# Kernel tuning notes

Hardware: AMD Instinct MI355X
Metric: run time of the kernel (lower is better)

## Reference

```python
import jax, jax.numpy as jnp
import numpy as np

SEQ, PREV, BS, D_IN, H, D = 512, 512, 8, 1024, 16, 64


def setup_inputs() -> dict:
    key = jax.random.key(0)
    ks = jax.random.split(key, 10)
    s = 0.02
    inp = {
        "input_": jax.random.normal(ks[0], (SEQ, BS, D_IN), jnp.float32),
        "pos_embs": jax.random.normal(ks[1], (SEQ + PREV, D_IN), jnp.float32),
        "memory": jax.random.normal(ks[2], (PREV, BS, D_IN), jnp.float32),
        "u": jax.random.normal(ks[3], (H, D), jnp.float32) * s,
        "v": jax.random.normal(ks[4], (H, D), jnp.float32) * s,
        # causal mask allowing full attention to memory: triu with diagonal=1+prev
        "mask": (jnp.triu(jnp.ones((SEQ, SEQ + PREV), jnp.bool_), k=1 + PREV))[..., None],
        "W_kv": jax.random.normal(ks[5], (D_IN, 2 * H * D), jnp.float32) * s,
        "W_q": jax.random.normal(ks[6], (D_IN, H * D), jnp.float32) * s,
        "W_p": jax.random.normal(ks[7], (D_IN, H * D), jnp.float32) * s,
        "W_out": jax.random.normal(ks[8], (H * D, D_IN), jnp.float32) * s,
        "ln_gamma": jnp.ones((D_IN,), jnp.float32),
        "ln_beta": jnp.zeros((D_IN,), jnp.float32),
    }
    return inp


def _rel_shift(x):
    # x: (q, k, bs, H) -> pad one zero column, reshape-transpose trick, drop first row
    q, k, bs, h = x.shape
    zp = jnp.zeros((q, 1, bs, h), x.dtype)
    return jnp.concatenate([zp, x], axis=1).reshape(k + 1, q, bs, h)[1:].reshape(q, k, bs, h)


def reference(input_, pos_embs, memory, u, v, mask, W_kv, W_q, W_p, W_out, ln_gamma, ln_beta):
    cur_seq, bs, d_in = input_.shape
    prev_seq = memory.shape[0]
    tot = cur_seq + prev_seq
    h, d = u.shape
    scale = 1.0 / d ** 0.5

    iwm = jnp.concatenate([memory, input_], axis=0)          # (tot, bs, d_in)
    kv = jnp.einsum('jbe,ef->jbf', iwm, W_kv)                 # (tot, bs, 2*H*d)
    k_t, v_t = jnp.split(kv, 2, axis=-1)
    q_t = jnp.einsum('ibe,ef->ibf', input_, W_q)              # (cur, bs, H*d)

    q4 = q_t.reshape(cur_seq, bs, h, d)
    k4 = k_t.reshape(tot, bs, h, d)
    v4 = v_t.reshape(tot, bs, h, d)

    content_attn = jnp.einsum('ibhd,jbhd->ijbh', q4 + u, k4)  # (cur, tot, bs, H)

    p_t = (pos_embs @ W_p).reshape(tot, h, d)                 # (tot, H, d)
    position_attn = jnp.einsum('ibhd,jhd->ijbh', q4 + v, p_t)
    position_attn = _rel_shift(position_attn)

    attn = content_attn + position_attn
    attn = jnp.where(mask[..., None], -jnp.inf, attn)         # mask: (cur, tot, 1) -> (cur, tot, 1, 1)
    attn = jax.nn.softmax(attn * scale, axis=1)

    awv = jnp.einsum('ijbh,jbhd->ibhd', attn, v4).reshape(cur_seq, bs, h * d)
    out = input_ + awv @ W_out                                # residual

    mu = jnp.mean(out, axis=-1, keepdims=True)
    var = jnp.mean((out - mu) ** 2, axis=-1, keepdims=True)
    out = (out - mu) / jnp.sqrt(var + 1e-5) * ln_gamma + ln_beta
    return out
```

## Files before the change

kernel.cpp:

```cpp
#include <hip/hip_runtime.h>
#include <math.h>

#define SEQ  512
#define PREV 512
#define TOT  1024
#define BSZ  8
#define DIN  1024
#define NH   16
#define HD   64

typedef __bf16 bf16;
typedef __bf16 bf16x8 __attribute__((ext_vector_type(8)));
typedef float  f32x4  __attribute__((ext_vector_type(4)));
typedef float  f32x16 __attribute__((ext_vector_type(16)));
typedef unsigned int u32;
typedef u32 u32x2 __attribute__((ext_vector_type(2)));

__device__ __forceinline__ f32x4 MFMA16(bf16x8 a, bf16x8 b, f32x4 c) {
    return __builtin_amdgcn_mfma_f32_16x16x32_bf16(a, b, c, 0, 0, 0);
}
__device__ __forceinline__ f32x16 MFMA32(bf16x8 a, bf16x8 b, f32x16 c) {
    return __builtin_amdgcn_mfma_f32_32x32x16_bf16(a, b, c, 0, 0, 0);
}

#define GLOAD16(g, l) __builtin_amdgcn_global_load_lds( \
    (const __attribute__((address_space(1))) void*)(g), \
    (__attribute__((address_space(3))) void*)(l), 16, 0, 0)

__device__ __forceinline__ unsigned short bfbits(float x) {
    return __builtin_bit_cast(unsigned short, (bf16)x);
}
__device__ __forceinline__ float bf2f(u32 bits16) {
    return __builtin_bit_cast(float, bits16 << 16);
}
__device__ __forceinline__ float exp2_raw(float x) {
    float r;
    asm("v_exp_f32 %0, %1" : "=v"(r) : "v"(x));
    return r;
}

__global__ __launch_bounds__(256) void prep_all(
    const float* __restrict__ memory, const float* __restrict__ input_,
    const float* __restrict__ pos,
    const float* __restrict__ W_kv, const float* __restrict__ W_q,
    const float* __restrict__ W_p,  const float* __restrict__ W_out,
    bf16* __restrict__ iwm, bf16* __restrict__ posb,
    bf16* __restrict__ wkv, bf16* __restrict__ wq,
    bf16* __restrict__ wp,  bf16* __restrict__ wo)
{
    __shared__ float tile[32][33];
    const int bid = blockIdx.x;
    const int t = threadIdx.x;
    if (bid < 9216) {
        const float* src; bf16* dst; int e4;
        if (bid < 8192) {
            e4 = (bid * 256 + t) * 4;
            src = (e4 < 4194304) ? memory : input_ - 4194304;
            dst = iwm;
        } else {
            e4 = ((bid - 8192) * 256 + t) * 4;
            src = pos; dst = posb;
        }
        float4 x = *(const float4*)(src + e4);
        union { bf16 h[4]; ushort4 u4; } pk;
        pk.h[0] = (bf16)x.x; pk.h[1] = (bf16)x.y; pk.h[2] = (bf16)x.z; pk.h[3] = (bf16)x.w;
        *(ushort4*)(dst + e4) = pk.u4;
        return;
    }
    const int rem = bid - 9216;
    const int bx = rem % 160, by = rem / 160;
    const float* W; bf16* Wt; int N, bn;
    if (bx < 64)       { W = W_kv;  Wt = wkv; N = 2048; bn = bx * 32; }
    else if (bx < 96)  { W = W_q;   Wt = wq;  N = 1024; bn = (bx - 64) * 32; }
    else if (bx < 128) { W = W_p;   Wt = wp;  N = 1024; bn = (bx - 96) * 32; }
    else               { W = W_out; Wt = wo;  N = 1024; bn = (bx - 128) * 32; }
    const int bk = by * 32;
    const int r = t >> 3, c4 = (t & 7) * 4;
    float4 x = *(const float4*)(W + (size_t)(bk + r) * N + bn + c4);
    tile[r][c4 + 0] = x.x; tile[r][c4 + 1] = x.y;
    tile[r][c4 + 2] = x.z; tile[r][c4 + 3] = x.w;
    __syncthreads();
    union { bf16 h[4]; ushort4 u4; } pk;
#pragma unroll
    for (int i = 0; i < 4; ++i) pk.h[i] = (bf16)tile[c4 + i][r];
    *(ushort4*)(Wt + (size_t)(bn + r) * 1024 + bk + c4) = pk.u4;
}

__global__ __launch_bounds__(256, 1) void gemm_kv(
    const bf16* __restrict__ A, const bf16* __restrict__ Bt,
    bf16* __restrict__ C, int M, int N, int K)
{
    __shared__ __align__(16) bf16 A_s[2][256 * 64];
    __shared__ __align__(16) bf16 B_s[2][256 * 64];
    const int t = threadIdx.x;
    const int w = t >> 6, lane = t & 63;
    const int ql = lane & 31, hi2 = lane >> 5;
    const int wm = w >> 1, wn = w & 1;
    const int lin = blockIdx.y * 8 + blockIdx.x;
    const int xcd = lin & 7, idx = lin >> 3;
    const int bm = (xcd * 4 + (idx & 3)) * 256;
    const int bn = (idx >> 2) * 256;

    f32x16 acc[4][4];
#pragma unroll
    for (int mf = 0; mf < 4; ++mf)
#pragma unroll
        for (int nf = 0; nf < 4; ++nf) acc[mf][nf] = (f32x16){};

    const int l7 = lane & 7, l3 = lane >> 3;

    auto stage_half = [&](int buf, int ks, int h) {
        const bf16* __restrict__ src = (h < 2) ? A : Bt;
        const int base = (h < 2) ? bm : bn;
        const int hh = (h & 1) * 128;
        bf16* dst = (h < 2) ? &A_s[buf][0] : &B_s[buf][0];
        const int k0 = ks << 6;
#pragma unroll
        for (int g = 0; g < 4; ++g) {
            const int row = hh + g * 32 + 8 * w + l3;
            const bf16* gp = src + (size_t)(base + row) * K + k0 + ((l7 ^ (row & 7)) * 8);
            GLOAD16(gp, dst + (size_t)row * 64 + l7 * 8);
        }
    };

    bf16x8 af[2][4], bfr[2][4];
    auto LDA = [&](int buf, int kt, int set) {
#pragma unroll
        for (int mf = 0; mf < 4; ++mf) {
            int row = wm * 128 + mf * 32 + ql;
            af[set][mf] = *(const bf16x8*)&A_s[buf][(size_t)row * 64 + (((kt * 2 + hi2) ^ (row & 7)) * 8)];
        }
    };
    auto LDB = [&](int buf, int kt, int set) {
#pragma unroll
        for (int nf = 0; nf < 4; ++nf) {
            int row = wn * 128 + nf * 32 + ql;
            bfr[set][nf] = *(const bf16x8*)&B_s[buf][(size_t)row * 64 + (((kt * 2 + hi2) ^ (row & 7)) * 8)];
        }
    };

    stage_half(0, 0, 0); stage_half(0, 0, 1); stage_half(0, 0, 2); stage_half(0, 0, 3);

    const int nk = K >> 6;
    for (int ks = 0; ks < nk; ++ks) {
        const int cur = ks & 1, nxt = cur ^ 1;
        asm volatile("s_waitcnt vmcnt(0)" ::: "memory");
        __builtin_amdgcn_sched_barrier(0);
        __builtin_amdgcn_s_barrier();
        __builtin_amdgcn_sched_barrier(0);
        LDA(cur, 0, 0); LDB(cur, 0, 0);
        if (ks + 1 < nk) {
            stage_half(nxt, ks + 1, 0); stage_half(nxt, ks + 1, 1);
            stage_half(nxt, ks + 1, 2); stage_half(nxt, ks + 1, 3);
        }
#pragma unroll
        for (int kt = 0; kt < 4; ++kt) {
            const int set = kt & 1;
            if (kt < 3) {
                LDA(cur, kt + 1, set ^ 1); LDB(cur, kt + 1, set ^ 1);
                asm volatile("s_waitcnt lgkmcnt(8)" ::: "memory");
            } else {
                asm volatile("s_waitcnt lgkmcnt(0)" ::: "memory");
            }
            __builtin_amdgcn_sched_barrier(0);
            __builtin_amdgcn_s_setprio(1);
#pragma unroll
            for (int mf = 0; mf < 4; ++mf)
#pragma unroll
                for (int nf = 0; nf < 4; ++nf)
                    acc[mf][nf] = MFMA32(af[set][mf], bfr[set][nf], acc[mf][nf]);
            __builtin_amdgcn_s_setprio(0);
        }
    }

#pragma unroll
    for (int mf = 0; mf < 4; ++mf)
#pragma unroll
        for (int nf = 0; nf < 4; ++nf)
#pragma unroll
            for (int r = 0; r < 16; ++r) {
                int row = bm + wm * 128 + mf * 32 + (r & 3) + 8 * (r >> 2) + 4 * hi2;
                int col = bn + wn * 128 + nf * 32 + ql;
                C[(size_t)row * N + col] = (bf16)acc[mf][nf][r];
            }
}

__global__ __launch_bounds__(256) void gemm_out(
    const bf16* __restrict__ A, const bf16* __restrict__ Bt,
    const float* __restrict__ Rres, float* __restrict__ Cf, int N, int K)
{
    __shared__ __align__(16) bf16 A_s[2][128 * 64];
    __shared__ __align__(16) bf16 B_s[2][128 * 64];
    const int t = threadIdx.x;
    const int w = t >> 6, lane = t & 63;
    const int li = lane & 15, hi = lane >> 4;
    const int wr = w >> 1, wc = w & 1;
    const int bm = blockIdx.y * 128, bn = blockIdx.x * 128;
    const int l3 = lane >> 3, l7 = lane & 7;
    const int srcoct = ((l7 ^ l3) * 8);

    f32x4 acc[4][4];
#pragma unroll
    for (int m = 0; m < 4; ++m)
#pragma unroll
        for (int n = 0; n < 4; ++n) acc[m][n] = (f32x4){0.f, 0.f, 0.f, 0.f};

    auto stage = [&](int buf, int k0) {
#pragma unroll
        for (int i = 0; i < 4; ++i) {
            int c = w * 4 + i;
            GLOAD16(A + (size_t)(bm + c * 8 + l3) * K + k0 + srcoct, &A_s[buf][c * 512]);
            GLOAD16(Bt + (size_t)(bn + c * 8 + l3) * K + k0 + srcoct, &B_s[buf][c * 512]);
        }
    };

    stage(0, 0);
    const int nk = K >> 6;
    for (int ks = 0; ks < nk; ++ks) {
        const int cur = ks & 1, nxt = cur ^ 1;
        asm volatile("s_waitcnt vmcnt(0)" ::: "memory");
        __builtin_amdgcn_sched_barrier(0);
        __builtin_amdgcn_s_barrier();
        __builtin_amdgcn_sched_barrier(0);
        if (ks + 1 < nk) stage(nxt, (ks + 1) << 6);
#pragma unroll
        for (int kk = 0; kk < 2; ++kk) {
            bf16x8 af[4], bfr[4];
#pragma unroll
            for (int m = 0; m < 4; ++m) {
                int row = wr * 64 + m * 16 + li;
                af[m] = *(const bf16x8*)&A_s[cur][row * 64 + ((kk * 32 + hi * 8) ^ ((row & 7) * 8))];
            }
#pragma unroll
            for (int n = 0; n < 4; ++n) {
                int row = wc * 64 + n * 16 + li;
                bfr[n] = *(const bf16x8*)&B_s[cur][row * 64 + ((kk * 32 + hi * 8) ^ ((row & 7) * 8))];
            }
            asm volatile("s_waitcnt lgkmcnt(0)" ::: "memory");
            __builtin_amdgcn_sched_barrier(0);
            __builtin_amdgcn_s_setprio(1);
#pragma unroll
            for (int m = 0; m < 4; ++m)
#pragma unroll
                for (int n = 0; n < 4; ++n)
                    acc[m][n] = MFMA16(af[m], bfr[n], acc[m][n]);
            __builtin_amdgcn_s_setprio(0);
        }
    }

#pragma unroll
    for (int m = 0; m < 4; ++m)
#pragma unroll
        for (int n = 0; n < 4; ++n)
#pragma unroll
            for (int r = 0; r < 4; ++r) {
                int row = bm + wr * 64 + m * 16 + hi * 4 + r;
                int col = bn + wc * 64 + n * 16 + li;
                size_t off = (size_t)row * N + col;
                Cf[off] = acc[m][n][r] + Rres[off];
            }
}

__global__ __launch_bounds__(256) void gemm_qp(
    const bf16* __restrict__ iwmq, const bf16* __restrict__ posb,
    const bf16* __restrict__ wq, const bf16* __restrict__ wp,
    bf16* __restrict__ qbf, bf16* __restrict__ pbf)
{
    __shared__ __align__(16) bf16 A_s[128 * 64];
    __shared__ __align__(16) bf16 B_s[128 * 64];
    const int t = threadIdx.x;
    const int w = t >> 6, lane = t & 63;
    const int li = lane & 15, hi = lane >> 4;
    const int wr = w >> 1, wc = w & 1;
    const int by = blockIdx.y;
    const bf16* A; const bf16* Bt; bf16* Cb; int bm;
    if (by < 32) { A = iwmq; Bt = wq; Cb = qbf; bm = by * 128; }
    else         { A = posb; Bt = wp; Cb = pbf; bm = (by - 32) * 128; }
    const int bn = blockIdx.x * 128;
    const int l3 = lane >> 3, l7 = lane & 7;
    const int srcoct = ((l7 ^ l3) * 8);

    f32x4 acc[4][4];
#pragma unroll
    for (int m = 0; m < 4; ++m)
#pragma unroll
        for (int n = 0; n < 4; ++n) acc[m][n] = (f32x4){0.f, 0.f, 0.f, 0.f};

    auto stage = [&](int k0) {
#pragma unroll
        for (int i = 0; i < 4; ++i) {
            int c = w * 4 + i;
            GLOAD16(A + (size_t)(bm + c * 8 + l3) * 1024 + k0 + srcoct, &A_s[c * 512]);
            GLOAD16(Bt + (size_t)(bn + c * 8 + l3) * 1024 + k0 + srcoct, &B_s[c * 512]);
        }
    };

    stage(0);
    for (int ks = 0; ks < 16; ++ks) {
        __syncthreads();
#pragma unroll
        for (int kk = 0; kk < 2; ++kk) {
            bf16x8 af[4], bfr[4];
#pragma unroll
            for (int m = 0; m < 4; ++m) {
                int row = wr * 64 + m * 16 + li;
                af[m] = *(const bf16x8*)&A_s[row * 64 + ((kk * 32 + hi * 8) ^ ((row & 7) * 8))];
            }
#pragma unroll
            for (int n = 0; n < 4; ++n) {
                int row = wc * 64 + n * 16 + li;
                bfr[n] = *(const bf16x8*)&B_s[row * 64 + ((kk * 32 + hi * 8) ^ ((row & 7) * 8))];
            }
#pragma unroll
            for (int m = 0; m < 4; ++m)
#pragma unroll
                for (int n = 0; n < 4; ++n)
                    acc[m][n] = MFMA16(af[m], bfr[n], acc[m][n]);
        }
        __syncthreads();
        if (ks + 1 < 16) stage((ks + 1) << 6);
    }

#pragma unroll
    for (int m = 0; m < 4; ++m)
#pragma unroll
        for (int n = 0; n < 4; ++n)
#pragma unroll
            for (int r = 0; r < 4; ++r) {
                int row = bm + wr * 64 + m * 16 + hi * 4 + r;
                int col = bn + wc * 64 + n * 16 + li;
                Cb[(size_t)row * 1024 + col] = (bf16)acc[m][n][r];
            }
}

__global__ __launch_bounds__(256, 2) void attn_mfma(
    const bf16* __restrict__ kv, const bf16* __restrict__ qb,
    const bf16* __restrict__ pb, const float* __restrict__ u,
    const float* __restrict__ v, bf16* __restrict__ awv)
{
    const int bi = (blockIdx.z & 1) ? (3 - blockIdx.x) : blockIdx.x;
    const int i0 = bi * 128;
    const int b  = blockIdx.y;
    const int h  = blockIdx.z;
    const int t  = threadIdx.x;
    const int w  = t >> 6;
    const int lane = t & 63;
    const int ql  = lane & 31;
    const int hi2 = lane >> 5;

    __shared__ __align__(16) bf16 K_s[64 * 64];
    __shared__ __align__(16) bf16 V_s[64][72];
    __shared__ __align__(16) bf16 P_s[256 * 64];
    __shared__ __align__(16) char SCR[4][6912];

    char* rsc = SCR[w];

    const int c8 = t & 7;
    const int rq = t >> 3;
    const int nt = 2 * bi + 10;
    const int C0 = 384 - i0;
    const float SCL2 = 0.125f * 1.44269504088896f;

    bf16x8 vreg[2];
#pragma unroll
    for (int p = 0; p < 2; ++p)
        vreg[p] = *(const bf16x8*)(kv + (size_t)((p * 32 + rq) * BSZ + b) * 2048 + 1024 + h * HD + c8 * 8);
#pragma unroll
    for (int p = 0; p < 2; ++p)
        GLOAD16(kv + (size_t)((p * 32 + rq) * BSZ + b) * 2048 + h * HD + ((c8 ^ (rq & 7)) * 8),
                K_s + (p * 32 + rq) * 64 + c8 * 8);
#pragma unroll
    for (int cp = 0; cp < 6; ++cp) {
        int grow = C0 + cp * 32 + rq;
        GLOAD16(pb + (size_t)grow * DIN + h * HD + ((c8 ^ (rq & 7)) * 8),
                P_s + (grow & 255) * 64 + c8 * 8);
    }

    bf16x8 qu[4], qv[4];
    {
        const size_t qoff = ((size_t)(i0 + w * 32 + ql) * BSZ + b) * DIN + h * HD;
#pragma unroll
        for (int kk = 0; kk < 4; ++kk) {
            bf16x8 q8 = *(const bf16x8*)(qb + qoff + kk * 16 + hi2 * 8);
            const float* up = u + h * HD + kk * 16 + hi2 * 8;
            const float* vp = v + h * HD + kk * 16 + hi2 * 8;
#pragma unroll
            for (int m = 0; m < 8; ++m) {
                float qf = (float)q8[m];
                qu[kk][m] = (bf16)(qf + up[m]);
                qv[kk][m] = (bf16)(qf + vp[m]);
            }
        }
    }

    float mrun = -1e30f, lrun = 0.f;
    f32x16 o[2];
    o[0] = (f32x16){}; o[1] = (f32x16){};

    const int phq = (31 - ql) & 3;
    const int sel = phq >> 1;
    const int shb = (phq & 1) * 16;

    for (int tt = 0; tt < nt; ++tt) {
        const int j0 = tt * 64;

        __builtin_amdgcn_s_barrier();
        __builtin_amdgcn_sched_barrier(0);

#pragma unroll
        for (int p = 0; p < 2; ++p) {
            int j = p * 32 + rq;
#pragma unroll
            for (int mm = 0; mm < 8; ++mm)
                V_s[c8 * 8 + mm][(j + 8 * c8) & 63] = vreg[p][mm];
        }
        asm volatile("s_waitcnt vmcnt(0) lgkmcnt(0)" ::: "memory");
        __builtin_amdgcn_sched_barrier(0);
        __builtin_amdgcn_s_barrier();
        __builtin_amdgcn_sched_barrier(0);

        f32x16 st[2];
        st[0] = (f32x16){}; st[1] = (f32x16){};
        __builtin_amdgcn_s_setprio(1);
#pragma unroll
        for (int jt = 0; jt < 2; ++jt) {
            int row = jt * 32 + ql;
#pragma unroll
            for (int kk = 0; kk < 4; ++kk) {
                bf16x8 kf = *(const bf16x8*)&K_s[row * 64 + (((kk * 2 + hi2) ^ (ql & 7)) * 8)];
                st[jt] = MFMA32(kf, qu[kk], st[jt]);
            }
        }
        const int bwg = j0 - i0 + 480 - 32 * w;
        f32x16 rp[3];
        rp[0] = (f32x16){}; rp[1] = (f32x16){}; rp[2] = (f32x16){};
#pragma unroll
        for (int Rt = 0; Rt < 3; ++Rt) {
            int ring = (bwg + Rt * 32 + ql) & 255;
#pragma unroll
            for (int kk = 0; kk < 4; ++kk) {
                bf16x8 pf = *(const bf16x8*)&P_s[ring * 64 + (((kk * 2 + hi2) ^ (ring & 7)) * 8)];
                rp[Rt] = MFMA32(pf, qv[kk], rp[Rt]);
            }
        }
        __builtin_amdgcn_s_setprio(0);

#pragma unroll
        for (int Rt = 0; Rt < 3; ++Rt)
#pragma unroll
            for (int a = 0; a < 4; ++a) {
                u32 lo = (u32)bfbits(rp[Rt][a * 4 + 0]) | ((u32)bfbits(rp[Rt][a * 4 + 1]) << 16);
                u32 hi = (u32)bfbits(rp[Rt][a * 4 + 2]) | ((u32)bfbits(rp[Rt][a * 4 + 3]) << 16);
                *(u32x2*)(rsc + ql * 216 + 64 * Rt + 16 * a + 8 * hi2) = (u32x2){lo, hi};
            }

        __builtin_amdgcn_s_barrier();
        __builtin_amdgcn_sched_barrier(0);

        if (tt + 1 < nt) {
            const int j0n = j0 + 64;
#pragma unroll
            for (int p = 0; p < 2; ++p)
                vreg[p] = *(const bf16x8*)(kv + (size_t)((j0n + p * 32 + rq) * BSZ + b) * 2048 + 1024 + h * HD + c8 * 8);
#pragma unroll
            for (int p = 0; p < 2; ++p)
                GLOAD16(kv + (size_t)((j0n + p * 32 + rq) * BSZ + b) * 2048 + h * HD + ((c8 ^ (rq & 7)) * 8),
                        K_s + (p * 32 + rq) * 64 + c8 * 8);
        }
        if (tt + 3 < nt) {
            const int Cs = C0 + (tt + 3) * 64;
#pragma unroll
            for (int p = 0; p < 2; ++p) {
                int grow = Cs + p * 32 + rq;
                GLOAD16(pb + (size_t)grow * DIN + h * HD + ((c8 ^ (rq & 7)) * 8),
                        P_s + (grow & 255) * 64 + c8 * 8);
            }
        }

        float rowmax = -1e30f;
        const int limb = i0 + 32 * w + ql + PREV - j0;
        auto assemble = [&](bool domask) {
#pragma unroll
            for (int jt = 0; jt < 2; ++jt)
#pragma unroll
                for (int a = 0; a < 4; ++a) {
                    int e = jt * 32 + 8 * a + 4 * hi2 + 31 - ql;
                    const u32x2* W = (const u32x2*)(rsc + ql * 216 + 8 * (e >> 2));
                    u32x2 A0 = W[0], A1 = W[1];
                    u32 U0 = sel ? A0[1] : A0[0];
                    u32 U1 = sel ? A1[0] : A0[1];
                    u32 U2 = sel ? A1[1] : A1[0];
                    u32 o0 = (u32)((((unsigned long long)U1 << 32) | U0) >> shb);
                    u32 o1 = (u32)((((unsigned long long)U2 << 32) | U1) >> shb);
                    float pq[4] = {bf2f(o0 & 0xffffu), bf2f(o0 >> 16),
                                   bf2f(o1 & 0xffffu), bf2f(o1 >> 16)};
#pragma unroll
                    for (int rr = 0; rr < 4; ++rr) {
                        int r = a * 4 + rr;
                        int lj = jt * 32 + 8 * a + 4 * hi2 + rr;
                        float sv = (st[jt][r] + pq[rr]) * SCL2;
                        if (domask && lj > limb) sv = -1e30f;
                        st[jt][r] = sv;
                        rowmax = fmaxf(rowmax, sv);
                    }
                }
        };
        if (__builtin_amdgcn_readfirstlane(j0 + 63 - (i0 + 32 * w + PREV)) > 0)
            assemble(true);
        else
            assemble(false);

        {
            u32 rm = __builtin_bit_cast(u32, rowmax), rm2 = rm;
            asm("v_permlane32_swap_b32 %0, %1" : "+v"(rm), "+v"(rm2));
            rowmax = fmaxf(rowmax, __builtin_bit_cast(float, rm));
            rowmax = fmaxf(rowmax, __builtin_bit_cast(float, rm2));
        }

        if (!__all(rowmax - mrun <= 11.54f)) {
            float newm = fmaxf(mrun, rowmax);
            float fsc = exp2_raw(mrun - newm);
#pragma unroll
            for (int r = 0; r < 16; ++r) {
                float fr = __shfl(fsc, (r & 3) + 8 * (r >> 2) + 4 * hi2);
                o[0][r] *= fr; o[1][r] *= fr;
            }
            lrun *= fsc;
            mrun = newm;
        }
        float rowsum = 0.f;
#pragma unroll
        for (int jt = 0; jt < 2; ++jt)
#pragma unroll
            for (int r = 0; r < 16; ++r) {
                float p = exp2_raw(st[jt][r] - mrun);
                st[jt][r] = p;
                rowsum += p;
            }
        {
            u32 rs = __builtin_bit_cast(u32, rowsum), rs2 = rs;
            asm("v_permlane32_swap_b32 %0, %1" : "+v"(rs), "+v"(rs2));
            rowsum += __builtin_bit_cast(float, rs2);
        }
        lrun += rowsum;

        u32 pk0[2][4], pk1[2][4];
#pragma unroll
        for (int jt = 0; jt < 2; ++jt)
#pragma unroll
            for (int a = 0; a < 4; ++a) {
                pk0[jt][a] = (u32)bfbits(st[jt][a * 4 + 0]) | ((u32)bfbits(st[jt][a * 4 + 1]) << 16);
                pk1[jt][a] = (u32)bfbits(st[jt][a * 4 + 2]) | ((u32)bfbits(st[jt][a * 4 + 3]) << 16);
            }

        __builtin_amdgcn_s_setprio(1);
#pragma unroll
        for (int js = 0; js < 4; ++js) {
            const int jt = js >> 1, a0 = 2 * (js & 1), a1 = a0 + 1;
            u32 w0 = pk0[jt][a0], w2 = pk0[jt][a1];
            asm("v_permlane32_swap_b32 %0, %1" : "+v"(w0), "+v"(w2));
            u32 w1 = pk1[jt][a0], w3 = pk1[jt][a1];
            asm("v_permlane32_swap_b32 %0, %1" : "+v"(w1), "+v"(w3));
            union { u32 uw[4]; bf16x8 vv; } pa;
            pa.uw[0] = w0; pa.uw[1] = w1; pa.uw[2] = w2; pa.uw[3] = w3;
#pragma unroll
            for (int dt = 0; dt < 2; ++dt) {
                int dcol = dt * 32 + ql;
                int colb = (js * 16 + hi2 * 8 + 8 * (dcol >> 3)) & 63;
                bf16x8 vf = *(const bf16x8*)&V_s[dcol][colb];
                o[dt] = MFMA32(pa.vv, vf, o[dt]);
            }
        }
        __builtin_amdgcn_s_setprio(0);
    }

    float linv = __builtin_amdgcn_rcpf(lrun);
    float lr[16];
#pragma unroll
    for (int r = 0; r < 16; ++r) lr[r] = __shfl(linv, (r & 3) + 8 * (r >> 2) + 4 * hi2);
#pragma unroll
    for (int dt = 0; dt < 2; ++dt)
#pragma unroll
        for (int r = 0; r < 16; ++r) {
            int row = i0 + 32 * w + (r & 3) + 8 * (r >> 2) + 4 * hi2;
            awv[((size_t)row * BSZ + b) * DIN + h * HD + dt * 32 + ql] = (bf16)(o[dt][r] * lr[r]);
        }
}

__global__ __launch_bounds__(256) void ln_f32(
    float* __restrict__ out, const float* __restrict__ gamma, const float* __restrict__ beta)
{
    const int row = blockIdx.x;
    const int t = threadIdx.x;
    float4 x = *(float4*)(out + (size_t)row * DIN + t * 4);
    float s  = x.x + x.y + x.z + x.w;
    float ss = x.x * x.x + x.y * x.y + x.z * x.z + x.w * x.w;
#pragma unroll
    for (int wd = 1; wd < 64; wd <<= 1) { s += __shfl_xor(s, wd); ss += __shfl_xor(ss, wd); }
    __shared__ float sbuf[4], ssbuf[4];
    const int wave = t >> 6, lanei = t & 63;
    if (lanei == 0) { sbuf[wave] = s; ssbuf[wave] = ss; }
    __syncthreads();
    s  = sbuf[0] + sbuf[1] + sbuf[2] + sbuf[3];
    ss = ssbuf[0] + ssbuf[1] + ssbuf[2] + ssbuf[3];
    const float mu   = s * (1.f / DIN);
    const float var  = ss * (1.f / DIN) - mu * mu;
    const float rstd = rsqrtf(var + 1e-5f);
    float4 g  = *(const float4*)(gamma + t * 4);
    float4 bb = *(const float4*)(beta + t * 4);
    float4 y;
    y.x = (x.x - mu) * rstd * g.x + bb.x;
    y.y = (x.y - mu) * rstd * g.y + bb.y;
    y.z = (x.z - mu) * rstd * g.z + bb.z;
    y.w = (x.w - mu) * rstd * g.w + bb.w;
    *(float4*)(out + (size_t)row * DIN + t * 4) = y;
}

extern "C" void kernel_launch(void* const* d_in, const int* in_sizes, int n_in,
                              void* d_out, int out_size, void* d_ws, size_t ws_size,
                              hipStream_t stream)
{
    const float* input_ = (const float*)d_in[0];
    const float* pos    = (const float*)d_in[1];
    const float* memory = (const float*)d_in[2];
    const float* u      = (const float*)d_in[3];
    const float* v      = (const float*)d_in[4];
    const float* W_kv   = (const float*)d_in[6];
    const float* W_q    = (const float*)d_in[7];
    const float* W_p    = (const float*)d_in[8];
    const float* W_out  = (const float*)d_in[9];
    const float* gamma  = (const float*)d_in[10];
    const float* beta   = (const float*)d_in[11];

    bf16* iwm  = (bf16*)d_ws;
    bf16* kvb  = iwm  + (size_t)8192 * 1024;
    bf16* qbf  = kvb  + (size_t)8192 * 2048;
    bf16* pbf  = qbf  + (size_t)4096 * 1024;
    bf16* posb = pbf  + (size_t)1024 * 1024;
    bf16* wkv  = posb + (size_t)1024 * 1024;
    bf16* wq   = wkv  + (size_t)2048 * 1024;
    bf16* wp   = wq   + (size_t)1024 * 1024;
    bf16* wo   = wp   + (size_t)1024 * 1024;
    bf16* awvb = wo   + (size_t)1024 * 1024;
    float* outf = (float*)d_out;

    prep_all<<<14336, 256, 0, stream>>>(memory, input_, pos, W_kv, W_q, W_p, W_out,
                                        iwm, posb, wkv, wq, wp, wo);

    gemm_kv<<<dim3(8, 32), 256, 0, stream>>>(iwm, wkv, kvb, 8192, 2048, 1024);
    gemm_qp<<<dim3(8, 40), 256, 0, stream>>>(iwm + (size_t)4096 * 1024, posb, wq, wp, qbf, pbf);

    attn_mfma<<<dim3(4, 8, 16), 256, 0, stream>>>(kvb, qbf, pbf, u, v, awvb);

    gemm_out<<<dim3(8, 32), 256, 0, stream>>>(awvb, wo, input_, outf, 1024, 1024);
    ln_f32<<<4096, 256, 0, stream>>>(outf, gamma, beta);
}
```

Before: 170.0 us.

## Merge KV, Q and P projection GEMMs into one triple-buffered 512-thread kernel

Replaces the separate gemm_kv and gemm_qp launches with a single gemm_proj kernel of 336 blocks. Each block computes a 256x256 tile with 8 waves, using 16x16 MFMAs and K-steps of 32 staged through a 3-deep LDS ring with partial vmcnt waits. The aim is to fill the GPU in one wave of blocks, drop a launch and the tail between the two GEMMs, and overlap global loads better. The cost is smaller K-steps, more barriers per unit of work, and higher register pressure from a 32-fragment accumulator at 2 blocks per CU.

New measurement: 192.7 us. 13.3% more time.

```diff
diff --git a/kernel.cpp b/kernel.cpp
--- a/kernel.cpp
+++ b/kernel.cpp
@@ -86,102 +86,104 @@
     *(ushort4*)(Wt + (size_t)(bn + r) * 1024 + bk + c4) = pk.u4;
 }
 
-__global__ __launch_bounds__(256, 1) void gemm_kv(
-    const bf16* __restrict__ A, const bf16* __restrict__ Bt,
-    bf16* __restrict__ C, int M, int N, int K)
+__global__ __launch_bounds__(512, 2) void gemm_proj(
+    const bf16* __restrict__ iwm, const bf16* __restrict__ posb,
+    const bf16* __restrict__ wkv, const bf16* __restrict__ wq,
+    const bf16* __restrict__ wp,
+    bf16* __restrict__ kvb, bf16* __restrict__ qbf, bf16* __restrict__ pbf)
 {
-    __shared__ __align__(16) bf16 A_s[2][256 * 64];
-    __shared__ __align__(16) bf16 B_s[2][256 * 64];
+    __shared__ __align__(16) bf16 A_s[3][256 * 32];
+    __shared__ __align__(16) bf16 B_s[3][256 * 32];
     const int t = threadIdx.x;
     const int w = t >> 6, lane = t & 63;
-    const int ql = lane & 31, hi2 = lane >> 5;
-    const int wm = w >> 1, wn = w & 1;
-    const int lin = blockIdx.y * 8 + blockIdx.x;
-    const int xcd = lin & 7, idx = lin >> 3;
-    const int bm = (xcd * 4 + (idx & 3)) * 256;
-    const int bn = (idx >> 2) * 256;
-
-    f32x16 acc[4][4];
-#pragma unroll
-    for (int mf = 0; mf < 4; ++mf)
-#pragma unroll
-        for (int nf = 0; nf < 4; ++nf) acc[mf][nf] = (f32x16){};
-
-    const int l7 = lane & 7, l3 = lane >> 3;
-
-    auto stage_half = [&](int buf, int ks, int h) {
-        const bf16* __restrict__ src = (h < 2) ? A : Bt;
-        const int base = (h < 2) ? bm : bn;
-        const int hh = (h & 1) * 128;
-        bf16* dst = (h < 2) ? &A_s[buf][0] : &B_s[buf][0];
-        const int k0 = ks << 6;
-#pragma unroll
-        for (int g = 0; g < 4; ++g) {
-            const int row = hh + g * 32 + 8 * w + l3;
-            const bf16* gp = src + (size_t)(base + row) * K + k0 + ((l7 ^ (row & 7)) * 8);
-            GLOAD16(gp, dst + (size_t)row * 64 + l7 * 8);
+    const int li = lane & 15, hi = lane >> 4;
+    const int wm = w >> 2, wn = w & 3;
+
+    const int lin = blockIdx.x;
+    const bf16* A; const bf16* Bt; bf16* C; int bm, bn, N;
+    if (lin < 256) {
+        const int xcd = lin & 7, idx = lin >> 3;
+        bm = (xcd * 4 + (idx & 3)) * 256;
+        bn = (idx >> 2) * 256;
+        A = iwm; Bt = wkv; C = kvb; N = 2048;
+    } else if (lin < 320) {
+        const int l = lin - 256;
+        bm = (l >> 2) * 256; bn = (l & 3) * 256;
+        A = iwm + (size_t)4096 * 1024; Bt = wq; C = qbf; N = 1024;
+    } else {
+        const int l = lin - 320;
+        bm = (l >> 2) * 256; bn = (l & 3) * 256;
+        A = posb; Bt = wp; C = pbf; N = 1024;
+    }
+
+    f32x4 acc[8][4];
+#pragma unroll
+    for (int m = 0; m < 8; ++m)
+#pragma unroll
+        for (int n = 0; n < 4; ++n) acc[m][n] = (f32x4){0.f, 0.f, 0.f, 0.f};
+
+    auto stage = [&](int buf, int kt) {
+        const int k0 = kt * 32;
+#pragma unroll
+        for (int e = 0; e < 2; ++e) {
+            const int f = e * 512 + t;
+            const int r = f >> 2, o = f & 3;
+            GLOAD16(A + (size_t)(bm + r) * 1024 + k0 + ((o ^ (r & 3)) * 8),
+                    &A_s[buf][f * 8]);
+        }
+#pragma unroll
+        for (int e = 0; e < 2; ++e) {
+            const int f = e * 512 + t;
+            const int r = f >> 2, o = f & 3;
+            GLOAD16(Bt + (size_t)(bn + r) * 1024 + k0 + ((o ^ (r & 3)) * 8),
+                    &B_s[buf][f * 8]);
         }
     };
 
-    bf16x8 af[2][4], bfr[2][4];
-    auto LDA = [&](int buf, int kt, int set) {
-#pragma unroll
-        for (int mf = 0; mf < 4; ++mf) {
-            int row = wm * 128 + mf * 32 + ql;
-            af[set][mf] = *(const bf16x8*)&A_s[buf][(size_t)row * 64 + (((kt * 2 + hi2) ^ (row & 7)) * 8)];
-        }
-    };
-    auto LDB = [&](int buf, int kt, int set) {
-#pragma unroll
-        for (int nf = 0; nf < 4; ++nf) {
-            int row = wn * 128 + nf * 32 + ql;
-            bfr[set][nf] = *(const bf16x8*)&B_s[buf][(size_t)row * 64 + (((kt * 2 + hi2) ^ (row & 7)) * 8)];
-        }
-    };
-
-    stage_half(0, 0, 0); stage_half(0, 0, 1); stage_half(0, 0, 2); stage_half(0, 0, 3);
-
-    const int nk = K >> 6;
-    for (int ks = 0; ks < nk; ++ks) {
-        const int cur = ks & 1, nxt = cur ^ 1;
-        asm volatile("s_waitcnt vmcnt(0)" ::: "memory");
+    stage(0, 0);
+    stage(1, 1);
+
+    const int nk = 32;
+    for (int kt = 0; kt < nk; ++kt) {
+        const int bc = kt % 3;
+        if (kt < nk - 1) { asm volatile("s_waitcnt vmcnt(4)" ::: "memory"); }
+        else             { asm volatile("s_waitcnt vmcnt(0)" ::: "memory"); }
         __builtin_amdgcn_sched_barrier(0);
         __builtin_amdgcn_s_barrier();
         __builtin_amdgcn_sched_barrier(0);
-        LDA(cur, 0, 0); LDB(cur, 0, 0);
-        if (ks + 1 < nk) {
-            stage_half(nxt, ks + 1, 0); stage_half(nxt, ks + 1, 1);
-            stage_half(nxt, ks + 1, 2); stage_half(nxt, ks + 1, 3);
-        }
-#pragma unroll
-        for (int kt = 0; kt < 4; ++kt) {
-            const int set = kt & 1;
-            if (kt < 3) {
-                LDA(cur, kt + 1, set ^ 1); LDB(cur, kt + 1, set ^ 1);
-                asm volatile("s_waitcnt lgkmcnt(8)" ::: "memory");
-            } else {
-                asm volatile("s_waitcnt lgkmcnt(0)" ::: "memory");
-            }
-            __builtin_amdgcn_sched_barrier(0);
-            __builtin_amdgcn_s_setprio(1);
-#pragma unroll
-            for (int mf = 0; mf < 4; ++mf)
-#pragma unroll
-                for (int nf = 0; nf < 4; ++nf)
-                    acc[mf][nf] = MFMA32(af[set][mf], bfr[set][nf], acc[mf][nf]);
-            __builtin_amdgcn_s_setprio(0);
-        }
-    }
-
-#pragma unroll
-    for (int mf = 0; mf < 4; ++mf)
-#pragma unroll
-        for (int nf = 0; nf < 4; ++nf)
-#pragma unroll
-            for (int r = 0; r < 16; ++r) {
-                int row = bm + wm * 128 + mf * 32 + (r & 3) + 8 * (r >> 2) + 4 * hi2;
-                int col = bn + wn * 128 + nf * 32 + ql;
-                C[(size_t)row * N + col] = (bf16)acc[mf][nf][r];
+        if (kt + 2 < nk) stage((kt + 2) % 3, kt + 2);
+
+        bf16x8 af[8], bfr[4];
+#pragma unroll
+        for (int m = 0; m < 8; ++m) {
+            int row = wm * 128 + m * 16 + li;
+            af[m] = *(const bf16x8*)&A_s[bc][row * 32 + ((hi ^ (row & 3)) * 8)];
+        }
+#pragma unroll
+        for (int n = 0; n < 4; ++n) {
+            int row = wn * 64 + n * 16 + li;
+            bfr[n] = *(const bf16x8*)&B_s[bc][row * 32 + ((hi ^ (row & 3)) * 8)];
+        }
+        asm volatile("s_waitcnt lgkmcnt(0)" ::: "memory");
+        __builtin_amdgcn_sched_barrier(0);
+        __builtin_amdgcn_s_setprio(1);
+#pragma unroll
+        for (int m = 0; m < 8; ++m)
+#pragma unroll
+            for (int n = 0; n < 4; ++n)
+                acc[m][n] = MFMA16(af[m], bfr[n], acc[m][n]);
+        __builtin_amdgcn_s_setprio(0);
+    }
+
+#pragma unroll
+    for (int m = 0; m < 8; ++m)
+#pragma unroll
+        for (int n = 0; n < 4; ++n)
+#pragma unroll
+            for (int r = 0; r < 4; ++r) {
+                int row = bm + wm * 128 + m * 16 + hi * 4 + r;
+                int col = bn + wn * 64 + n * 16 + li;
+                C[(size_t)row * N + col] = (bf16)acc[m][n][r];
             }
 }
 
@@ -258,78 +260,6 @@
                 int col = bn + wc * 64 + n * 16 + li;
                 size_t off = (size_t)row * N + col;
                 Cf[off] = acc[m][n][r] + Rres[off];
-            }
-}
-
-__global__ __launch_bounds__(256) void gemm_qp(
-    const bf16* __restrict__ iwmq, const bf16* __restrict__ posb,
-    const bf16* __restrict__ wq, const bf16* __restrict__ wp,
-    bf16* __restrict__ qbf, bf16* __restrict__ pbf)
-{
-    __shared__ __align__(16) bf16 A_s[128 * 64];
-    __shared__ __align__(16) bf16 B_s[128 * 64];
-    const int t = threadIdx.x;
-    const int w = t >> 6, lane = t & 63;
-    const int li = lane & 15, hi = lane >> 4;
-    const int wr = w >> 1, wc = w & 1;
-    const int by = blockIdx.y;
-    const bf16* A; const bf16* Bt; bf16* Cb; int bm;
-    if (by < 32) { A = iwmq; Bt = wq; Cb = qbf; bm = by * 128; }
-    else         { A = posb; Bt = wp; Cb = pbf; bm = (by - 32) * 128; }
-    const int bn = blockIdx.x * 128;
-    const int l3 = lane >> 3, l7 = lane & 7;
-    const int srcoct = ((l7 ^ l3) * 8);
-
-    f32x4 acc[4][4];
-#pragma unroll
-    for (int m = 0; m < 4; ++m)
-#pragma unroll
-        for (int n = 0; n < 4; ++n) acc[m][n] = (f32x4){0.f, 0.f, 0.f, 0.f};
-
-    auto stage = [&](int k0) {
-#pragma unroll
-        for (int i = 0; i < 4; ++i) {
-            int c = w * 4 + i;
-            GLOAD16(A + (size_t)(bm + c * 8 + l3) * 1024 + k0 + srcoct, &A_s[c * 512]);
-            GLOAD16(Bt + (size_t)(bn + c * 8 + l3) * 1024 + k0 + srcoct, &B_s[c * 512]);
-        }
-    };
-
-    stage(0);
-    for (int ks = 0; ks < 16; ++ks) {
-        __syncthreads();
-#pragma unroll
-        for (int kk = 0; kk < 2; ++kk) {
-            bf16x8 af[4], bfr[4];
-#pragma unroll
-            for (int m = 0; m < 4; ++m) {
-                int row = wr * 64 + m * 16 + li;
-                af[m] = *(const bf16x8*)&A_s[row * 64 + ((kk * 32 + hi * 8) ^ ((row & 7) * 8))];
-            }
-#pragma unroll
-            for (int n = 0; n < 4; ++n) {
-                int row = wc * 64 + n * 16 + li;
-                bfr[n] = *(const bf16x8*)&B_s[row * 64 + ((kk * 32 + hi * 8) ^ ((row & 7) * 8))];
-            }
-#pragma unroll
-            for (int m = 0; m < 4; ++m)
-#pragma unroll
-                for (int n = 0; n < 4; ++n)
-                    acc[m][n] = MFMA16(af[m], bfr[n], acc[m][n]);
-        }
-        __syncthreads();
-        if (ks + 1 < 16) stage((ks + 1) << 6);
-    }
-
-#pragma unroll
-    for (int m = 0; m < 4; ++m)
-#pragma unroll
-        for (int n = 0; n < 4; ++n)
-#pragma unroll
-            for (int r = 0; r < 4; ++r) {
-                int row = bm + wr * 64 + m * 16 + hi * 4 + r;
-                int col = bn + wc * 64 + n * 16 + li;
-                Cb[(size_t)row * 1024 + col] = (bf16)acc[m][n][r];
             }
 }
 
@@ -647,8 +577,7 @@
     prep_all<<<14336, 256, 0, stream>>>(memory, input_, pos, W_kv, W_q, W_p, W_out,
                                         iwm, posb, wkv, wq, wp, wo);
 
-    gemm_kv<<<dim3(8, 32), 256, 0, stream>>>(iwm, wkv, kvb, 8192, 2048, 1024);
-    gemm_qp<<<dim3(8, 40), 256, 0, stream>>>(iwm + (size_t)4096 * 1024, posb, wq, wp, qbf, pbf);
+    gemm_proj<<<336, 512, 0, stream>>>(iwm, posb, wkv, wq, wp, kvb, qbf, pbf);
 
     attn_mfma<<<dim3(4, 8, 16), 256, 0, stream>>>(kvb, qbf, pbf, u, v, awvb);
 
```
